# Optimization experiments

Hardware: AMD Instinct MI355X
Metric: run time of the kernel (lower is better)

Reference implementation:

```python
import jax, jax.numpy as jnp
import numpy as np

N = 100000
E = 3200000
IN_DIM, HID, MLP_HID, K = 3, 64, 128, 15


def setup_inputs() -> dict:
    key = jax.random.key(0)
    ks = jax.random.split(key, 10)
    x = jax.random.normal(ks[0], (N, IN_DIM), dtype=jnp.float32)
    edge_index = jax.random.randint(ks[1], (2, E), 0, N, dtype=jnp.int32)
    def glorot(k, shape):
        lim = float(np.sqrt(6.0 / (shape[0] + shape[1])))
        return jax.random.uniform(k, shape, jnp.float32, -lim, lim)
    return {
        "x": x,
        "edge_index": edge_index,
        "W1": glorot(ks[2], (IN_DIM, HID)), "b1": jnp.zeros((HID,), jnp.float32),
        "W2": glorot(ks[3], (HID, HID)),    "b2": jnp.zeros((HID,), jnp.float32),
        "Wm1": glorot(ks[4], (HID, MLP_HID)), "bm1": jnp.zeros((MLP_HID,), jnp.float32),
        "Wm2": glorot(ks[5], (MLP_HID, K)),   "bm2": jnp.zeros((K,), jnp.float32),
    }


def _gcn_layer(h, W, b, src, dst, deg_inv_sqrt, n):
    # h: [N, Fin] -> [N, Fout]; GCNConv: D^-1/2 (A+I) D^-1/2 (h W) + b
    hw = h @ W  # dense GEMM first (Fin small)
    norm = deg_inv_sqrt[src] * deg_inv_sqrt[dst]  # [E+N]
    msg = hw[src] * norm[:, None]                 # irregular gather, [E+N, Fout]
    out = jax.ops.segment_sum(msg, dst, num_segments=n)  # scatter-add
    return out + b


def reference(x, edge_index, W1, b1, W2, b2, Wm1, bm1, Wm2, bm2):
    n = x.shape[0]
    loops = jnp.arange(n, dtype=edge_index.dtype)
    src = jnp.concatenate([edge_index[0], loops])  # self-loops appended
    dst = jnp.concatenate([edge_index[1], loops])
    deg = jax.ops.segment_sum(jnp.ones_like(dst, dtype=x.dtype), dst, num_segments=n)
    deg_inv_sqrt = jnp.where(deg > 0, jax.lax.rsqrt(jnp.maximum(deg, 1.0)), 0.0)

    h = jax.nn.elu(_gcn_layer(x, W1, b1, src, dst, deg_inv_sqrt, n))
    h = jax.nn.elu(_gcn_layer(h, W2, b2, src, dst, deg_inv_sqrt, n))
    # MLP (dropout is identity in eval mode)
    h = jax.nn.elu(h @ Wm1 + bm1)
    H = h @ Wm2 + bm2
    return jax.nn.softmax(H, axis=1)  # [N, K]
```

## Files before the change

### kernel.cpp

```cpp
#include <hip/hip_runtime.h>
#include <hip/hip_fp16.h>
#include <math.h>


#define SPAN 128
#define CAPP 6400
#define CAPC 4608
#define CH   8192
#define EPT  16
#define H2P  88
#define MSP2 136

typedef _Float16 v8hf __attribute__((ext_vector_type(8)));
typedef float    v4f  __attribute__((ext_vector_type(4)));

__device__ __forceinline__ float elu(float v) { return v > 0.f ? v : expm1f(v); }

__global__ __launch_bounds__(512) void scatter_kernel(const int* __restrict__ src,
    const int* __restrict__ dst, int* __restrict__ cursor, unsigned* __restrict__ colb,
    const float* __restrict__ W2, const float* __restrict__ Wm1,
    const float* __restrict__ Wm2, __half* __restrict__ W2t,
    __half* __restrict__ Wm1t, __half* __restrict__ Wm2p,
    __half* __restrict__ s1h, __half* __restrict__ sxh,
    int E, int NBK, int nChunks, int N) {
    int tid = threadIdx.x;
    if ((int)blockIdx.x == nChunks) {
        for (int i = tid; i < 64 * 64; i += 512) {
            int f = i >> 6, k = i & 63;
            W2t[f * 64 + k] = __float2half(W2[k * 64 + f]);
        }
        for (int i = tid; i < 128 * 64; i += 512) {
            int j = i >> 6, f = i & 63;
            Wm1t[j * 64 + f] = __float2half(Wm1[f * 128 + j]);
        }
        for (int i = tid; i < 4 * 64 * 8; i += 512) {
            int j = i & 7, l = (i >> 3) & 63, t = i >> 9;
            int k = t * 32 + (l >> 4) * 8 + j;
            int c = l & 15;
            Wm2p[i] = (c < 15) ? __float2half(Wm2[k * 15 + c]) : __half(0.f);
        }
        if (tid < 32) {
            ((uint2*)(s1h + (size_t)N * 64))[tid & 15] = uint2{0u, 0u};
            if (tid == 16) *((uint2*)(sxh + (size_t)N * 4)) = uint2{0u, 0u};
        }
        return;
    }
    __shared__ int hist[1024];
    __shared__ unsigned gb[1024];
    int chunk = blockIdx.x;
    for (int i = tid; i < NBK; i += 512) hist[i] = 0;
    __syncthreads();
    int base = chunk * CH;
    int cnt = min(CH, E - base);
    unsigned br[EPT], dt[EPT];
#pragma unroll
    for (int j = 0; j < EPT; ++j) {
        int idx = j * 512 + tid;
        br[j] = 0xFFFFFFFFu;
        if (idx < cnt) {
            int e = base + idx;
            int s = src[e], d = dst[e];
            int b = d >> 7;
            int r = atomicAdd(&hist[b], 1);
            br[j] = ((unsigned)b << 13) | (unsigned)r;
            dt[j] = ((unsigned)(d & 127) << 17) | (unsigned)s;
        }
    }
    __syncthreads();
    for (int b = tid; b < NBK; b += 512) {
        int c = hist[b];
        gb[b] = (unsigned)(b * CAPP) + (c ? (unsigned)atomicAdd(&cursor[b], c) : 0u);
    }
    __syncthreads();
#pragma unroll
    for (int j = 0; j < EPT; ++j) {
        if (br[j] != 0xFFFFFFFFu) {
            int b = br[j] >> 13;
            int r = br[j] & 8191;
            unsigned pos = gb[b] + (unsigned)r;
            if (pos < (unsigned)(b + 1) * CAPP) colb[pos] = dt[j];
        }
    }
}

__global__ __launch_bounds__(512) void csr_sort_kernel(unsigned* __restrict__ colb,
    const int* __restrict__ cursor, const float* __restrict__ x,
    uint2* __restrict__ rp2, float* __restrict__ dis, __half* __restrict__ sxh,
    int N) {
    __shared__ __align__(16) unsigned ebuf[CAPC];
    __shared__ __align__(16) int sbuf[CAPC];
    __shared__ int cnt[SPAN], offC[SPAN], offP[SPAN], fill[SPAN];
    int b = blockIdx.x, tid = threadIdx.x;
    int n = min(cursor[b], CAPC);
    size_t base = (size_t)b * CAPP;
    if (tid < SPAN) cnt[tid] = 0;
    int n4 = n >> 2;
    for (int k = tid; k < n4; k += 512)
        *(uint4*)(ebuf + 4 * k) = *(const uint4*)(colb + base + 4 * k);
    for (int i = (n4 << 2) + tid; i < n; i += 512) ebuf[i] = colb[base + i];
    __syncthreads();
    for (int i = tid; i < n; i += 512) atomicAdd(&cnt[(ebuf[i] >> 17) & 127], 1);
    __syncthreads();
    if (tid < 64) {
        int n0 = b * SPAN + tid, n1 = n0 + 64;
        int c0 = cnt[tid], c1 = cnt[tid + 64];
        int sc0 = (n0 < N) ? c0 : 0;
        int sc1 = (n1 < N) ? c1 : 0;
        int sp0 = (n0 < N) ? ((c0 + 16) & ~15) : 0;
        int sp1 = (n1 < N) ? ((c1 + 16) & ~15) : 0;
        int a0 = sc0, a1 = sc1, p0 = sp0, p1 = sp1;
#pragma unroll
        for (int off = 1; off < 64; off <<= 1) {
            int t0 = __shfl_up(a0, off), t1 = __shfl_up(a1, off);
            int u0 = __shfl_up(p0, off), u1 = __shfl_up(p1, off);
            if (tid >= off) { a0 += t0; a1 += t1; p0 += u0; p1 += u1; }
        }
        int totC = __shfl(a0, 63), totP = __shfl(p0, 63);
        offC[tid]      = a0 - sc0;
        offC[tid + 64] = totC + a1 - sc1;
        offP[tid]      = p0 - sp0;
        offP[tid + 64] = totP + p1 - sp1;
    }
    __syncthreads();
    if (tid < SPAN) {
        fill[tid] = offC[tid];
        int node = b * SPAN + tid;
        if (node < N) {
            int c = cnt[tid];
            uint2 rp;
            rp.x = (unsigned)(base + offP[tid]);
            rp.y = rp.x + (unsigned)c + 1u;
            rp2[node] = rp;
            float r = rsqrtf((float)(c + 1));
            dis[node] = r;
            __half2 h0 = __floats2half2_rn(r * x[node * 3 + 0], r * x[node * 3 + 1]);
            __half2 h1 = __floats2half2_rn(r * x[node * 3 + 2], 0.f);
            uint2 w; w.x = *(unsigned*)&h0; w.y = *(unsigned*)&h1;
            *(uint2*)(sxh + (size_t)node * 4) = w;
        }
    }
    __syncthreads();
    for (int i = tid; i < n; i += 512) {
        unsigned e = ebuf[i];
        int pos = atomicAdd(&fill[(e >> 17) & 127], 1);
        sbuf[pos] = (int)(e & 0x1FFFF);
    }
    __syncthreads();
    int hw = tid >> 5, hl = tid & 31;
    for (int nd = hw; nd < SPAN; nd += 16) {
        int node = b * SPAN + nd;
        if (node >= N) continue;
        int c = cnt[nd], oc = offC[nd];
        unsigned gp = (unsigned)(base + offP[nd]);
        for (int j = hl; j < c; j += 32)
            colb[gp + j] = (unsigned)sbuf[oc + j];
        int pk = (c + 16) & ~15;
        for (int j = c + hl; j < pk; j += 32)
            colb[gp + j] = (j == c) ? (unsigned)node : (unsigned)N;
    }
}

__global__ void agg3_kernel(const __half* __restrict__ sxh, const uint2* __restrict__ rp2,
                            const unsigned* __restrict__ colb, const float* __restrict__ dis,
                            const float* __restrict__ W1, const float* __restrict__ b1,
                            __half* __restrict__ s1h, int N) {
    int wave = (blockIdx.x * blockDim.x + threadIdx.x) >> 6;
    int lane = threadIdx.x & 63;
    int hl = lane & 31;
    int d = wave * 2 + (lane >> 5);
    bool act = d < N;
    int start = 0, end = 0;
    if (act) { uint2 rp = rp2[d]; start = (int)rp.x; end = (int)rp.y; }
    float a0 = 0.f, a1 = 0.f, a2v = 0.f;
    for (int i = start + hl; i < end; i += 32) {
        uint2 rq = *(const uint2*)(sxh + (size_t)colb[i] * 4);
        float2 u0 = __half22float2(*(__half2*)&rq.x);
        float2 u1 = __half22float2(*(__half2*)&rq.y);
        a0 += u0.x; a1 += u0.y; a2v += u1.x;
    }
#pragma unroll
    for (int off = 16; off; off >>= 1) {
        a0  += __shfl_xor(a0, off);
        a1  += __shfl_xor(a1, off);
        a2v += __shfl_xor(a2v, off);
    }
    if (act) {
        float r = dis[d];
        float v0 = r * (a0 * W1[hl]      + a1 * W1[64 + hl]      + a2v * W1[128 + hl])      + b1[hl];
        float v1 = r * (a0 * W1[32 + hl] + a1 * W1[96 + hl]      + a2v * W1[160 + hl])      + b1[32 + hl];
        s1h[(size_t)d * 64 + hl]      = __float2half(r * elu(v0));
        s1h[(size_t)d * 64 + 32 + hl] = __float2half(r * elu(v1));
    }
}

__global__ void agg64_kernel(const __half* __restrict__ s1h, const uint2* __restrict__ rp2,
                             const unsigned* __restrict__ colb, const float* __restrict__ dis,
                             __half* __restrict__ a2h, int N) {
    int wave = (blockIdx.x * blockDim.x + threadIdx.x) >> 6;
    int lane = threadIdx.x & 63;
    int g = lane >> 3;
    int f = lane & 7;
    int d = wave;
    if (d >= N) return;
    uint2 rp = rp2[d];
    float r = dis[d];
    int start = (int)rp.x;
    int len = (int)(rp.y - rp.x);
    int pend = start + ((len + 15) & ~15);
    float acc0 = 0.f, acc1 = 0.f, acc2 = 0.f, acc3 = 0.f;
    float acc4 = 0.f, acc5 = 0.f, acc6 = 0.f, acc7 = 0.f;
    for (int i = start; i < pend; i += 16) {
        int ca = (int)colb[i + g];
        int cb = (int)colb[i + 8 + g];
        uint4 A = *(const uint4*)(s1h + (size_t)ca * 64 + f * 8);
        uint4 B = *(const uint4*)(s1h + (size_t)cb * 64 + f * 8);
        __half2 p0 = __hadd2(*(__half2*)&A.x, *(__half2*)&B.x);
        __half2 p1 = __hadd2(*(__half2*)&A.y, *(__half2*)&B.y);
        __half2 p2 = __hadd2(*(__half2*)&A.z, *(__half2*)&B.z);
        __half2 p3 = __hadd2(*(__half2*)&A.w, *(__half2*)&B.w);
        float2 q0 = __half22float2(p0);
        float2 q1 = __half22float2(p1);
        float2 q2 = __half22float2(p2);
        float2 q3 = __half22float2(p3);
        acc0 += q0.x; acc1 += q0.y; acc2 += q1.x; acc3 += q1.y;
        acc4 += q2.x; acc5 += q2.y; acc6 += q3.x; acc7 += q3.y;
    }
#pragma unroll
    for (int off = 8; off <= 32; off <<= 1) {
        acc0 += __shfl_xor(acc0, off);
        acc1 += __shfl_xor(acc1, off);
        acc2 += __shfl_xor(acc2, off);
        acc3 += __shfl_xor(acc3, off);
        acc4 += __shfl_xor(acc4, off);
        acc5 += __shfl_xor(acc5, off);
        acc6 += __shfl_xor(acc6, off);
        acc7 += __shfl_xor(acc7, off);
    }
    if (g == 0) {
        __half2 o0 = __floats2half2_rn(r * acc0, r * acc1);
        __half2 o1 = __floats2half2_rn(r * acc2, r * acc3);
        __half2 o2 = __floats2half2_rn(r * acc4, r * acc5);
        __half2 o3 = __floats2half2_rn(r * acc6, r * acc7);
        uint4 w;
        w.x = *(unsigned*)&o0; w.y = *(unsigned*)&o1;
        w.z = *(unsigned*)&o2; w.w = *(unsigned*)&o3;
        *(uint4*)(a2h + (size_t)d * 64 + f * 8) = w;
    }
}

__global__ __launch_bounds__(256) void h1_kernel(const __half* __restrict__ a2h,
    const __half* __restrict__ W2t, const float* __restrict__ b2g,
    const __half* __restrict__ Wm1t, const float* __restrict__ bm1g,
    const __half* __restrict__ Wm2p, const float* __restrict__ bm2g,
    float* __restrict__ out, int N) {
    __shared__ __align__(16) __half h2s[64 * H2P];
    __shared__ __align__(16) __half ms[64 * MSP2];
    int tid = threadIdx.x;
    int wave = tid >> 6, lane = tid & 63;
    int q = lane >> 4, l16 = lane & 15;
    int base = blockIdx.x * 64;

    v8hf wc[4];
#pragma unroll
    for (int t = 0; t < 4; ++t)
        wc[t] = *(const v8hf*)(Wm2p + ((size_t)(t * 64 + lane)) * 8);
    float bbc = (l16 < 15) ? bm2g[l16] : 0.f;

    {
        int nodeRow = base + wave * 16 + l16;
        size_t arow = (size_t)min(nodeRow, N - 1) * 64;
        v8hf af0 = *(const v8hf*)(a2h + arow + q * 8);
        v8hf af1 = *(const v8hf*)(a2h + arow + 32 + q * 8);
#pragma unroll
        for (int fb = 0; fb < 4; ++fb) {
            float bb = b2g[fb * 16 + l16];
            v4f acc = {bb, bb, bb, bb};
            v8hf b0 = *(const v8hf*)(W2t + (fb * 16 + l16) * 64 + q * 8);
            v8hf b1 = *(const v8hf*)(W2t + (fb * 16 + l16) * 64 + 32 + q * 8);
            acc = __builtin_amdgcn_mfma_f32_16x16x32_f16(af0, b0, acc, 0, 0, 0);
            acc = __builtin_amdgcn_mfma_f32_16x16x32_f16(af1, b1, acc, 0, 0, 0);
#pragma unroll
            for (int r = 0; r < 4; ++r)
                h2s[(wave * 16 + q * 4 + r) * H2P + fb * 16 + l16] =
                    __float2half(elu(acc[r]));
        }
    }
    __syncthreads();
    {
        int arow = (wave * 16 + l16) * H2P;
        v8hf af0 = *(const v8hf*)(h2s + arow + q * 8);
        v8hf af1 = *(const v8hf*)(h2s + arow + 32 + q * 8);
#pragma unroll
        for (int jb = 0; jb < 8; ++jb) {
            float bb = bm1g[jb * 16 + l16];
            v4f acc = {bb, bb, bb, bb};
            v8hf b0 = *(const v8hf*)(Wm1t + (jb * 16 + l16) * 64 + q * 8);
            v8hf b1 = *(const v8hf*)(Wm1t + (jb * 16 + l16) * 64 + 32 + q * 8);
            acc = __builtin_amdgcn_mfma_f32_16x16x32_f16(af0, b0, acc, 0, 0, 0);
            acc = __builtin_amdgcn_mfma_f32_16x16x32_f16(af1, b1, acc, 0, 0, 0);
#pragma unroll
            for (int r = 0; r < 4; ++r)
                ms[(wave * 16 + q * 4 + r) * MSP2 + jb * 16 + l16] =
                    __float2half(elu(acc[r]));
        }
    }
    __syncthreads();
    {
        int arow = (wave * 16 + l16) * MSP2;
        v4f accC = {bbc, bbc, bbc, bbc};
#pragma unroll
        for (int t = 0; t < 4; ++t) {
            v8hf a = *(const v8hf*)(ms + arow + t * 32 + q * 8);
            accC = __builtin_amdgcn_mfma_f32_16x16x32_f16(a, wc[t], accC, 0, 0, 0);
        }
#pragma unroll
        for (int r = 0; r < 4; ++r) {
            float lg = (l16 < 15) ? accC[r] : -1e30f;
            float mx = lg;
            mx = fmaxf(mx, __shfl_xor(mx, 1));
            mx = fmaxf(mx, __shfl_xor(mx, 2));
            mx = fmaxf(mx, __shfl_xor(mx, 4));
            mx = fmaxf(mx, __shfl_xor(mx, 8));
            float ex = (l16 < 15) ? __expf(lg - mx) : 0.f;
            float sden = ex;
            sden += __shfl_xor(sden, 1);
            sden += __shfl_xor(sden, 2);
            sden += __shfl_xor(sden, 4);
            sden += __shfl_xor(sden, 8);
            int node = base + wave * 16 + q * 4 + r;
            if (l16 < 15 && node < N)
                out[(size_t)node * 15 + l16] = ex / sden;
        }
    }
}

extern "C" void kernel_launch(void* const* d_in, const int* in_sizes, int n_in,
                              void* d_out, int out_size, void* d_ws, size_t ws_size,
                              hipStream_t stream) {
    const float* x   = (const float*)d_in[0];
    const int*   ei  = (const int*)d_in[1];
    const float* W1  = (const float*)d_in[2];
    const float* b1  = (const float*)d_in[3];
    const float* W2  = (const float*)d_in[4];
    const float* b2  = (const float*)d_in[5];
    const float* Wm1 = (const float*)d_in[6];
    const float* bm1 = (const float*)d_in[7];
    const float* Wm2 = (const float*)d_in[8];
    const float* bm2 = (const float*)d_in[9];
    float* out = (float*)d_out;

    int N = in_sizes[0] / 3;
    int E = in_sizes[1] / 2;
    const int* src = ei;
    const int* dst = ei + E;
    int NBK = (N + SPAN - 1) / SPAN;

    uintptr_t p = (uintptr_t)d_ws;
    auto carve = [&](size_t bytes) -> void* {
        p = (p + 255) & ~(uintptr_t)255;
        void* r = (void*)p;
        p += bytes;
        return r;
    };
    unsigned* colb    = (unsigned*)carve((size_t)NBK * CAPP * 4 + 256);
    __half*   a2h     = (__half*)carve((size_t)N * 64 * 2);
    __half*   s1h     = (__half*)carve((size_t)(N + 1) * 64 * 2);
    int*      cursor  = (int*)carve((size_t)NBK * 4);
    uint2*    rp2     = (uint2*)carve((size_t)N * 8);
    float*    dis     = (float*)carve((size_t)N * 4);
    __half*   sxh     = (__half*)carve((size_t)(N + 1) * 8);
    __half*   W2t     = (__half*)carve(64 * 64 * 2);
    __half*   Wm1t    = (__half*)carve(128 * 64 * 2);
    __half*   Wm2p    = (__half*)carve(4 * 64 * 8 * 2);

    int nChunks = (E + CH - 1) / CH;
    int aggBlocks = (N + 7) / 8;
    int aggBlocks64 = (N + 3) / 4;
    int nTiles = (N + 63) / 64;

    hipMemsetAsync(cursor, 0, (size_t)NBK * 4, stream);
    scatter_kernel<<<nChunks + 1, 512, 0, stream>>>(src, dst, cursor, colb,
        W2, Wm1, Wm2, W2t, Wm1t, Wm2p, s1h, sxh, E, NBK, nChunks, N);
    csr_sort_kernel<<<NBK, 512, 0, stream>>>(colb, cursor, x, rp2, dis, sxh, N);
    agg3_kernel<<<aggBlocks, 256, 0, stream>>>(sxh, rp2, colb, dis, W1, b1, s1h, N);
    agg64_kernel<<<aggBlocks64, 256, 0, stream>>>(s1h, rp2, colb, dis, a2h, N);
    h1_kernel<<<nTiles, 256, 0, stream>>>(a2h, W2t, b2, Wm1t, bm1, Wm2p, bm2, out, N);
}
```

Measured before the change: 235.5 us.

## Fuse layer-2 aggregation into MLP kernel via shared memory; vectorize CSR writes

Layer-2 neighbor aggregation now runs inside the MLP kernel. Each block gathers 64 nodes into LDS, so the a2h round-trip through global memory and one kernel launch go away. The CSR column writes in csr_sort are also vectorized to uint4 stores. In exchange, each wave now handles 16 nodes in sequence, which cuts the number of waves working on the latency-bound gather (1563 blocks instead of 25000). That loss of parallelism and latency hiding may outweigh the bandwidth saved.

```diff
diff --git a/kernel.cpp b/kernel.cpp
--- a/kernel.cpp
+++ b/kernel.cpp
@@ -10,6 +10,7 @@
 #define EPT  16
 #define H2P  88
 #define MSP2 136
+#define A2P  72
 
 typedef _Float16 v8hf __attribute__((ext_vector_type(8)));
 typedef float    v4f  __attribute__((ext_vector_type(4)));
@@ -152,11 +153,16 @@
         if (node >= N) continue;
         int c = cnt[nd], oc = offC[nd];
         unsigned gp = (unsigned)(base + offP[nd]);
-        for (int j = hl; j < c; j += 32)
-            colb[gp + j] = (unsigned)sbuf[oc + j];
-        int pk = (c + 16) & ~15;
-        for (int j = c + hl; j < pk; j += 32)
-            colb[gp + j] = (j == c) ? (unsigned)node : (unsigned)N;
+        int pk4 = ((c + 16) & ~15) >> 2;
+        for (int j4 = hl; j4 < pk4; j4 += 32) {
+            int j = j4 << 2;
+            uint4 v;
+            v.x = (j     < c) ? (unsigned)sbuf[oc + j]     : ((j     == c) ? (unsigned)node : (unsigned)N);
+            v.y = (j + 1 < c) ? (unsigned)sbuf[oc + j + 1] : ((j + 1 == c) ? (unsigned)node : (unsigned)N);
+            v.z = (j + 2 < c) ? (unsigned)sbuf[oc + j + 2] : ((j + 2 == c) ? (unsigned)node : (unsigned)N);
+            v.w = (j + 3 < c) ? (unsigned)sbuf[oc + j + 3] : ((j + 3 == c) ? (unsigned)node : (unsigned)N);
+            *(uint4*)(colb + gp + j) = v;
+        }
     }
 }
 
@@ -193,73 +199,76 @@
     }
 }
 
-__global__ void agg64_kernel(const __half* __restrict__ s1h, const uint2* __restrict__ rp2,
-                             const unsigned* __restrict__ colb, const float* __restrict__ dis,
-                             __half* __restrict__ a2h, int N) {
-    int wave = (blockIdx.x * blockDim.x + threadIdx.x) >> 6;
-    int lane = threadIdx.x & 63;
-    int g = lane >> 3;
-    int f = lane & 7;
-    int d = wave;
-    if (d >= N) return;
-    uint2 rp = rp2[d];
-    float r = dis[d];
-    int start = (int)rp.x;
-    int len = (int)(rp.y - rp.x);
-    int pend = start + ((len + 15) & ~15);
-    float acc0 = 0.f, acc1 = 0.f, acc2 = 0.f, acc3 = 0.f;
-    float acc4 = 0.f, acc5 = 0.f, acc6 = 0.f, acc7 = 0.f;
-    for (int i = start; i < pend; i += 16) {
-        int ca = (int)colb[i + g];
-        int cb = (int)colb[i + 8 + g];
-        uint4 A = *(const uint4*)(s1h + (size_t)ca * 64 + f * 8);
-        uint4 B = *(const uint4*)(s1h + (size_t)cb * 64 + f * 8);
-        __half2 p0 = __hadd2(*(__half2*)&A.x, *(__half2*)&B.x);
-        __half2 p1 = __hadd2(*(__half2*)&A.y, *(__half2*)&B.y);
-        __half2 p2 = __hadd2(*(__half2*)&A.z, *(__half2*)&B.z);
-        __half2 p3 = __hadd2(*(__half2*)&A.w, *(__half2*)&B.w);
-        float2 q0 = __half22float2(p0);
-        float2 q1 = __half22float2(p1);
-        float2 q2 = __half22float2(p2);
-        float2 q3 = __half22float2(p3);
-        acc0 += q0.x; acc1 += q0.y; acc2 += q1.x; acc3 += q1.y;
-        acc4 += q2.x; acc5 += q2.y; acc6 += q3.x; acc7 += q3.y;
-    }
-#pragma unroll
-    for (int off = 8; off <= 32; off <<= 1) {
-        acc0 += __shfl_xor(acc0, off);
-        acc1 += __shfl_xor(acc1, off);
-        acc2 += __shfl_xor(acc2, off);
-        acc3 += __shfl_xor(acc3, off);
-        acc4 += __shfl_xor(acc4, off);
-        acc5 += __shfl_xor(acc5, off);
-        acc6 += __shfl_xor(acc6, off);
-        acc7 += __shfl_xor(acc7, off);
-    }
-    if (g == 0) {
-        __half2 o0 = __floats2half2_rn(r * acc0, r * acc1);
-        __half2 o1 = __floats2half2_rn(r * acc2, r * acc3);
-        __half2 o2 = __floats2half2_rn(r * acc4, r * acc5);
-        __half2 o3 = __floats2half2_rn(r * acc6, r * acc7);
-        uint4 w;
-        w.x = *(unsigned*)&o0; w.y = *(unsigned*)&o1;
-        w.z = *(unsigned*)&o2; w.w = *(unsigned*)&o3;
-        *(uint4*)(a2h + (size_t)d * 64 + f * 8) = w;
-    }
-}
-
-__global__ __launch_bounds__(256) void h1_kernel(const __half* __restrict__ a2h,
+__global__ __launch_bounds__(256) void aggmlp_kernel(const __half* __restrict__ s1h,
+    const uint2* __restrict__ rp2, const unsigned* __restrict__ colb,
+    const float* __restrict__ dis,
     const __half* __restrict__ W2t, const float* __restrict__ b2g,
     const __half* __restrict__ Wm1t, const float* __restrict__ bm1g,
     const __half* __restrict__ Wm2p, const float* __restrict__ bm2g,
     float* __restrict__ out, int N) {
     __shared__ __align__(16) __half h2s[64 * H2P];
-    __shared__ __align__(16) __half ms[64 * MSP2];
+    __shared__ __align__(16) __half msb[64 * MSP2];
+    __half* a2s = msb;
     int tid = threadIdx.x;
     int wave = tid >> 6, lane = tid & 63;
+    int base = blockIdx.x * 64;
+    int g = lane >> 3;
+    int f = lane & 7;
+
+    for (int k = 0; k < 16; ++k) {
+        int local = wave * 16 + k;
+        int d = base + local;
+        float acc0 = 0.f, acc1 = 0.f, acc2 = 0.f, acc3 = 0.f;
+        float acc4 = 0.f, acc5 = 0.f, acc6 = 0.f, acc7 = 0.f;
+        float r = 0.f;
+        if (d < N) {
+            uint2 rp = rp2[d];
+            r = dis[d];
+            int start = (int)rp.x;
+            int len = (int)(rp.y - rp.x);
+            int pend = start + ((len + 15) & ~15);
+            for (int i = start; i < pend; i += 16) {
+                int ca = (int)colb[i + g];
+                int cb = (int)colb[i + 8 + g];
+                uint4 A = *(const uint4*)(s1h + (size_t)ca * 64 + f * 8);
+                uint4 B = *(const uint4*)(s1h + (size_t)cb * 64 + f * 8);
+                __half2 p0 = __hadd2(*(__half2*)&A.x, *(__half2*)&B.x);
+                __half2 p1 = __hadd2(*(__half2*)&A.y, *(__half2*)&B.y);
+                __half2 p2 = __hadd2(*(__half2*)&A.z, *(__half2*)&B.z);
+                __half2 p3 = __hadd2(*(__half2*)&A.w, *(__half2*)&B.w);
+                float2 q0 = __half22float2(p0);
+                float2 q1 = __half22float2(p1);
+                float2 q2 = __half22float2(p2);
+                float2 q3 = __half22float2(p3);
+                acc0 += q0.x; acc1 += q0.y; acc2 += q1.x; acc3 += q1.y;
+                acc4 += q2.x; acc5 += q2.y; acc6 += q3.x; acc7 += q3.y;
+            }
+        }
+#pragma unroll
+        for (int off = 8; off <= 32; off <<= 1) {
+            acc0 += __shfl_xor(acc0, off);
+            acc1 += __shfl_xor(acc1, off);
+            acc2 += __shfl_xor(acc2, off);
+            acc3 += __shfl_xor(acc3, off);
+            acc4 += __shfl_xor(acc4, off);
+            acc5 += __shfl_xor(acc5, off);
+            acc6 += __shfl_xor(acc6, off);
+            acc7 += __shfl_xor(acc7, off);
+        }
+        if (g == 0) {
+            __half2 o0 = __floats2half2_rn(r * acc0, r * acc1);
+            __half2 o1 = __floats2half2_rn(r * acc2, r * acc3);
+            __half2 o2 = __floats2half2_rn(r * acc4, r * acc5);
+            __half2 o3 = __floats2half2_rn(r * acc6, r * acc7);
+            uint4 w;
+            w.x = *(unsigned*)&o0; w.y = *(unsigned*)&o1;
+            w.z = *(unsigned*)&o2; w.w = *(unsigned*)&o3;
+            *(uint4*)(a2s + local * A2P + f * 8) = w;
+        }
+    }
+    __syncthreads();
+
     int q = lane >> 4, l16 = lane & 15;
-    int base = blockIdx.x * 64;
-
     v8hf wc[4];
 #pragma unroll
     for (int t = 0; t < 4; ++t)
@@ -267,10 +276,9 @@
     float bbc = (l16 < 15) ? bm2g[l16] : 0.f;
 
     {
-        int nodeRow = base + wave * 16 + l16;
-        size_t arow = (size_t)min(nodeRow, N - 1) * 64;
-        v8hf af0 = *(const v8hf*)(a2h + arow + q * 8);
-        v8hf af1 = *(const v8hf*)(a2h + arow + 32 + q * 8);
+        int arow = (wave * 16 + l16) * A2P;
+        v8hf af0 = *(const v8hf*)(a2s + arow + q * 8);
+        v8hf af1 = *(const v8hf*)(a2s + arow + 32 + q * 8);
 #pragma unroll
         for (int fb = 0; fb < 4; ++fb) {
             float bb = b2g[fb * 16 + l16];
@@ -300,7 +308,7 @@
             acc = __builtin_amdgcn_mfma_f32_16x16x32_f16(af1, b1, acc, 0, 0, 0);
 #pragma unroll
             for (int r = 0; r < 4; ++r)
-                ms[(wave * 16 + q * 4 + r) * MSP2 + jb * 16 + l16] =
+                msb[(wave * 16 + q * 4 + r) * MSP2 + jb * 16 + l16] =
                     __float2half(elu(acc[r]));
         }
     }
@@ -310,7 +318,7 @@
         v4f accC = {bbc, bbc, bbc, bbc};
 #pragma unroll
         for (int t = 0; t < 4; ++t) {
-            v8hf a = *(const v8hf*)(ms + arow + t * 32 + q * 8);
+            v8hf a = *(const v8hf*)(msb + arow + t * 32 + q * 8);
             accC = __builtin_amdgcn_mfma_f32_16x16x32_f16(a, wc[t], accC, 0, 0, 0);
         }
 #pragma unroll
@@ -363,7 +371,6 @@
         return r;
     };
     unsigned* colb    = (unsigned*)carve((size_t)NBK * CAPP * 4 + 256);
-    __half*   a2h     = (__half*)carve((size_t)N * 64 * 2);
     __half*   s1h     = (__half*)carve((size_t)(N + 1) * 64 * 2);
     int*      cursor  = (int*)carve((size_t)NBK * 4);
     uint2*    rp2     = (uint2*)carve((size_t)N * 8);
@@ -375,7 +382,6 @@
 
     int nChunks = (E + CH - 1) / CH;
     int aggBlocks = (N + 7) / 8;
-    int aggBlocks64 = (N + 3) / 4;
     int nTiles = (N + 63) / 64;
 
     hipMemsetAsync(cursor, 0, (size_t)NBK * 4, stream);
@@ -383,6 +389,6 @@
         W2, Wm1, Wm2, W2t, Wm1t, Wm2p, s1h, sxh, E, NBK, nChunks, N);
     csr_sort_kernel<<<NBK, 512, 0, stream>>>(colb, cursor, x, rp2, dis, sxh, N);
     agg3_kernel<<<aggBlocks, 256, 0, stream>>>(sxh, rp2, colb, dis, W1, b1, s1h, N);
-    agg64_kernel<<<aggBlocks64, 256, 0, stream>>>(s1h, rp2, colb, dis, a2h, N);
-    h1_kernel<<<nTiles, 256, 0, stream>>>(a2h, W2t, b2, Wm1t, bm1, Wm2p, bm2, out, N);
-}
+    aggmlp_kernel<<<nTiles, 256, 0, stream>>>(s1h, rp2, colb, dis,
+        W2t, b2, Wm1t, bm1, Wm2p, bm2, out, N);
+}
```

After: 261.4 us. +11.0%, slower.
